# Performance work log

Hardware: AMD Instinct MI355X
Metric: run time of the kernel (lower is better)

## Reference

```python
import jax, jax.numpy as jnp
import numpy as np

D_MODEL, D_STATE, EXPAND, D_CONV, HEADDIM = 1024, 128, 2, 4, 64
D_INNER = EXPAND * D_MODEL                      # 2048
NHEADS = D_INNER // HEADDIM                     # 32
NGROUPS = 1
CONV_DIM = D_INNER + 2 * NGROUPS * D_STATE      # 2304
D_IN_PROJ = 2 * D_INNER + 2 * NGROUPS * D_STATE + NHEADS  # 4384
BATCH, SEQ = 2, 4096
EPS = 1e-5


def setup_inputs() -> dict:
    key = jax.random.key(0)
    ks = jax.random.split(key, 6)
    sn = lambda k, shape, sc: jax.random.normal(k, shape, jnp.float32) * sc
    # dt_bias such that softplus(dt_bias) spans [1e-3, 0.1] (mamba2 init)
    dt = jnp.linspace(1e-3, 0.1, NHEADS)
    return {
        "x": sn(ks[0], (BATCH, SEQ, D_MODEL), 1.0),
        "ln_w": jnp.ones((D_MODEL,), jnp.float32),
        "ln_b": jnp.zeros((D_MODEL,), jnp.float32),
        "in_proj_w": sn(ks[1], (D_IN_PROJ, D_MODEL), D_MODEL ** -0.5),
        "conv_w": sn(ks[2], (CONV_DIM, D_CONV), D_CONV ** -0.5),
        "conv_b": jnp.zeros((CONV_DIM,), jnp.float32),
        "dt_bias": jnp.log(jnp.expm1(dt)).astype(jnp.float32),
        "A_log": jnp.log(jnp.arange(1, NHEADS + 1, dtype=jnp.float32)),
        "D": jnp.ones((NHEADS,), jnp.float32),
        "norm_w": jnp.ones((D_INNER,), jnp.float32),
        "out_proj_w": sn(ks[3], (D_MODEL, D_INNER), D_INNER ** -0.5),
    }


def _mamba2(u, in_proj_w, conv_w, conv_b, dt_bias, A_log, Dp, norm_w, out_proj_w):
    b, l, _ = u.shape
    zxbcdt = u @ in_proj_w.T                              # [b,l,4384]
    z, xBC, dt = jnp.split(zxbcdt, [D_INNER, D_INNER + CONV_DIM], axis=-1)
    # causal depthwise conv1d over channels, then SiLU
    xBC = jnp.transpose(xBC, (0, 2, 1))                   # [b,conv_dim,l]
    xBC = jax.lax.conv_general_dilated(
        xBC, conv_w[:, None, :], window_strides=(1,),
        padding=[(D_CONV - 1, 0)], feature_group_count=CONV_DIM,
        dimension_numbers=("NCH", "OIH", "NCH"))
    xBC = jax.nn.silu(jnp.transpose(xBC, (0, 2, 1)) + conv_b)
    x, Bm, Cm = jnp.split(xBC, [D_INNER, D_INNER + NGROUPS * D_STATE], axis=-1)
    dt = jax.nn.softplus(dt + dt_bias)                    # [b,l,h]
    A = -jnp.exp(A_log)                                   # [h]
    xh = x.reshape(b, l, NHEADS, HEADDIM)
    # time-major for the selective scan
    dt_t, x_t = jnp.moveaxis(dt, 1, 0), jnp.moveaxis(xh, 1, 0)
    B_t, C_t = jnp.moveaxis(Bm, 1, 0), jnp.moveaxis(Cm, 1, 0)

    def step(h, inputs):
        dtk, xk, Bk, Ck = inputs                          # [b,h],[b,h,p],[b,n],[b,n]
        decay = jnp.exp(dtk * A)                          # [b,h]
        h = h * decay[:, :, None, None] + (dtk[:, :, None, None] * xk[..., None]) * Bk[:, None, None, :]
        y = jnp.einsum("bhpn,bn->bhp", h, Ck)
        return h, y

    h0 = jnp.zeros((b, NHEADS, HEADDIM, D_STATE), u.dtype)
    _, ys = jax.lax.scan(step, h0, (dt_t, x_t, B_t, C_t))  # ys: [l,b,h,p]
    y = jnp.moveaxis(ys, 0, 1) + Dp[None, None, :, None] * xh
    y = y.reshape(b, l, D_INNER)
    # gated RMSNorm: rmsnorm(y * silu(z)) * norm_w
    y = y * jax.nn.silu(z)
    y = y * jax.lax.rsqrt(jnp.mean(y * y, axis=-1, keepdims=True) + EPS) * norm_w
    return y @ out_proj_w.T


def reference(x, ln_w, ln_b, in_proj_w, conv_w, conv_b, dt_bias, A_log, D, norm_w, out_proj_w):
    mu = jnp.mean(x, -1, keepdims=True)
    var = jnp.mean((x - mu) ** 2, -1, keepdims=True)
    xn = (x - mu) * jax.lax.rsqrt(var + EPS) * ln_w + ln_b
    # dropout is identity at inference
    return x + _mamba2(xn, in_proj_w, conv_w, conv_b, dt_bias, A_log, D, norm_w, out_proj_w)
```

## Files before the change

kernel.cpp:

```cpp
#include <hip/hip_runtime.h>
#include <cstdint>

#define D_MODEL 1024
#define D_INNER 2048
#define NHEADS 32
#define HEADDIM 64
#define D_STATE 128
#define CONV_DIM 2304
#define D_IN_PROJ 4384
#define SEQ 4096
#define NROWS 8192
#define NPROJ_PAD 4480
#define TCH 128
#define NCHUNK 32
#define CR 8

typedef float f32x4 __attribute__((ext_vector_type(4)));
typedef __bf16 bf16x8 __attribute__((ext_vector_type(8)));
typedef unsigned short u16;

__device__ __forceinline__ u16 f2bf(float f) {
  uint32_t u = __builtin_bit_cast(uint32_t, f);
  u += 0x7FFFu + ((u >> 16) & 1u);
  return (u16)(u >> 16);
}
__device__ __forceinline__ float bf2f(u16 h) {
  return __builtin_bit_cast(float, (uint32_t)h << 16);
}
__device__ __forceinline__ float dexp(float a) { return expf(fminf(0.f, a)); }

typedef __attribute__((address_space(1))) const void gv_t;
typedef __attribute__((address_space(3))) void lv_t;
__device__ __forceinline__ void gload_lds16(const void* g, void* l) {
  __builtin_amdgcn_global_load_lds((gv_t*)g, (lv_t*)l, 16, 0, 0);
}

__global__ __launch_bounds__(256) void cvt_pad(const float* __restrict__ s,
                                               u16* __restrict__ d, int n_src, int n_dst) {
  int i = (blockIdx.x * 256 + threadIdx.x) * 4;
  int stride = gridDim.x * 256 * 4;
  for (; i < n_dst; i += stride) {
    ushort4 o;
    if (i < n_src) {
      float4 v = *(const float4*)&s[i];
      o.x = f2bf(v.x); o.y = f2bf(v.y); o.z = f2bf(v.z); o.w = f2bf(v.w);
    } else {
      o.x = o.y = o.z = o.w = 0;
    }
    *(ushort4*)&d[i] = o;
  }
}

__global__ __launch_bounds__(256) void ln_kernel(const float* __restrict__ x,
                                                 const float* __restrict__ w,
                                                 const float* __restrict__ b,
                                                 u16* __restrict__ out) {
  int row = blockIdx.x, tid = threadIdx.x;
  const float4 v = *(const float4*)&x[(long)row * D_MODEL + tid * 4];
  float s1 = v.x + v.y + v.z + v.w;
  float s2 = v.x * v.x + v.y * v.y + v.z * v.z + v.w * v.w;
#pragma unroll
  for (int m = 32; m >= 1; m >>= 1) {
    s1 += __shfl_xor(s1, m);
    s2 += __shfl_xor(s2, m);
  }
  __shared__ float p1[4], p2[4];
  if ((tid & 63) == 0) { p1[tid >> 6] = s1; p2[tid >> 6] = s2; }
  __syncthreads();
  s1 = p1[0] + p1[1] + p1[2] + p1[3];
  s2 = p2[0] + p2[1] + p2[2] + p2[3];
  float mean = s1 * (1.f / D_MODEL);
  float var = s2 * (1.f / D_MODEL) - mean * mean;
  float rstd = rsqrtf(var + 1e-5f);
  const float4 wv = *(const float4*)&w[tid * 4];
  const float4 bv = *(const float4*)&b[tid * 4];
  ushort4 o;
  o.x = f2bf((v.x - mean) * rstd * wv.x + bv.x);
  o.y = f2bf((v.y - mean) * rstd * wv.y + bv.y);
  o.z = f2bf((v.z - mean) * rstd * wv.z + bv.z);
  o.w = f2bf((v.w - mean) * rstd * wv.w + bv.w);
  *(ushort4*)&out[(long)row * D_MODEL + tid * 4] = o;
}

template <int MODE>
__global__ __launch_bounds__(256, 4) void gemm_bt(const u16* __restrict__ A,
                                                  const u16* __restrict__ B, int K,
                                                  u16* __restrict__ zb,
                                                  u16* __restrict__ xb,
                                                  float* __restrict__ dtb,
                                                  float* __restrict__ C,
                                                  const float* __restrict__ resid) {
  __shared__ __align__(16) u16 As[128 * 64];
  __shared__ __align__(16) u16 Bs[128 * 64];
  const int tid = threadIdx.x;
  const int NB = gridDim.x;
  const int wg = (blockIdx.x & 7) * (NB >> 3) + (blockIdx.x >> 3);
  const int m0 = (wg & 63) * 128;
  const int n0 = (wg >> 6) * 128;
  const int w = tid >> 6, l = tid & 63;
  const int wm = w >> 1, wn = w & 1;

  f32x4 acc[4][4] = {};

  for (int k0 = 0; k0 < K; k0 += 64) {
#pragma unroll
    for (int i = 0; i < 4; ++i) {
      int idx = i * 256 + tid;
      int row = idx >> 3, slot = idx & 7;
      int ks = slot ^ (row & 7);
      const u16* ga = A + (long)(m0 + row) * K + k0 + ks * 8;
      gload_lds16(ga, (char*)As + idx * 16);
      const u16* gb = B + (long)(n0 + row) * K + k0 + ks * 8;
      gload_lds16(gb, (char*)Bs + idx * 16);
    }
    __syncthreads();
    bf16x8 af[2][4], bfr[2][4];
#pragma unroll
    for (int kk = 0; kk < 2; ++kk)
#pragma unroll
      for (int f = 0; f < 4; ++f) {
        int rowa = wm * 64 + f * 16 + (l & 15);
        int ca = ((kk << 2) | (l >> 4)) ^ (rowa & 7);
        af[kk][f] = *(const bf16x8*)((const char*)As + rowa * 128 + ca * 16);
        int rowb = wn * 64 + f * 16 + (l & 15);
        int cb2 = ((kk << 2) | (l >> 4)) ^ (rowb & 7);
        bfr[kk][f] = *(const bf16x8*)((const char*)Bs + rowb * 128 + cb2 * 16);
      }
#pragma unroll
    for (int kk = 0; kk < 2; ++kk)
#pragma unroll
      for (int mf = 0; mf < 4; ++mf)
#pragma unroll
        for (int nf = 0; nf < 4; ++nf)
          acc[mf][nf] = __builtin_amdgcn_mfma_f32_16x16x32_bf16(
              af[kk][mf], bfr[kk][nf], acc[mf][nf], 0, 0, 0);
    __syncthreads();
  }
#pragma unroll
  for (int mf = 0; mf < 4; ++mf)
#pragma unroll
    for (int nf = 0; nf < 4; ++nf) {
      int col = n0 + wn * 64 + nf * 16 + (l & 15);
#pragma unroll
      for (int r = 0; r < 4; ++r) {
        int rowm = m0 + wm * 64 + mf * 16 + (l >> 4) * 4 + r;
        float v = acc[mf][nf][r];
        if (MODE == 0) {
          if (col < D_INNER)
            zb[(long)rowm * D_INNER + col] = f2bf(v);
          else if (col < D_INNER + CONV_DIM)
            xb[(long)rowm * CONV_DIM + (col - D_INNER)] = f2bf(v);
          else if (col < D_IN_PROJ)
            dtb[(long)rowm * NHEADS + (col - D_INNER - CONV_DIM)] = v;
        } else {
          long off = (long)rowm * D_MODEL + col;
          C[off] = v + resid[off];
        }
      }
    }
}

__global__ __launch_bounds__(256) void conv_silu_kernel(const u16* __restrict__ xr,
                                                        const float* __restrict__ cw,
                                                        const float* __restrict__ cb,
                                                        u16* __restrict__ xp,
                                                        u16* __restrict__ bc) {
  const int c = blockIdx.x * 256 + threadIdx.x;
  const int row0 = blockIdx.y * CR;
  const int t0 = row0 & (SEQ - 1);
  const float4 wv = *(const float4*)&cw[c * 4];
  const float bias = cb[c];
  float xwin[CR + 3];
#pragma unroll
  for (int k = 0; k < CR + 3; ++k) {
    int t = t0 - 3 + k;
    xwin[k] = (t >= 0) ? bf2f(xr[(long)(row0 - 3 + k) * CONV_DIM + c]) : 0.f;
  }
#pragma unroll
  for (int j = 0; j < CR; ++j) {
    float a = bias + xwin[j] * wv.x + xwin[j + 1] * wv.y + xwin[j + 2] * wv.z +
              xwin[j + 3] * wv.w;
    a = a / (1.f + expf(-a));
    int row = row0 + j;
    if (c < D_INNER)
      xp[(long)row * D_INNER + c] = f2bf(a);
    else
      bc[(long)row * (2 * D_STATE) + (c - D_INNER)] = f2bf(a);
  }
}

__global__ __launch_bounds__(256, 2) void ssd_state_kernel(
    const u16* __restrict__ xp, const u16* __restrict__ bcb,
    const float* __restrict__ dtf, const float* __restrict__ dt_bias,
    const float* __restrict__ A_log, u16* __restrict__ S,
    float* __restrict__ cdk) {
  const int hh = blockIdx.x, cc = blockIdx.y, bb = blockIdx.z;
  const int tid = threadIdx.x, w = tid >> 6, l = tid & 63;
  __shared__ __align__(16) u16 Bs[128 * 128];
  __shared__ __align__(16) u16 WXs[128 * 64];
  __shared__ float ws[128];
  const long rowbase = (long)bb * SEQ + cc * TCH;
  const float Ah = -expf(A_log[hh]);
  const float dbias = dt_bias[hh];

#pragma unroll
  for (int i = 0; i < 8; ++i) {
    int idx = i * 256 + tid, t = idx >> 4, kb = idx & 15;
    int kbs = kb ^ (((t >> 3) & 3) << 1);
    gload_lds16(bcb + (rowbase + t) * 256 + kbs * 8, (char*)Bs + idx * 16);
  }
  if (w == 0) {
    float r0 = dtf[(rowbase + l) * NHEADS + hh] + dbias;
    float r1 = dtf[(rowbase + 64 + l) * NHEADS + hh] + dbias;
    float d0 = r0 > 20.f ? r0 : log1pf(expf(r0));
    float d1 = r1 > 20.f ? r1 : log1pf(expf(r1));
    float a0 = d0 * Ah, a1 = d1 * Ah;
#pragma unroll
    for (int d = 1; d < 64; d <<= 1) { float u = __shfl_up(a0, d); if (l >= d) a0 += u; }
#pragma unroll
    for (int d = 1; d < 64; d <<= 1) { float u = __shfl_up(a1, d); if (l >= d) a1 += u; }
    float t0 = __shfl(a0, 63);
    float tot = __shfl(a1, 63) + t0;
    ws[l] = dexp(tot - a0) * d0;
    ws[64 + l] = dexp(tot - (a1 + t0)) * d1;
    if (l == 0) cdk[(bb * 32 + hh) * NCHUNK + cc] = dexp(tot);
  }
  __syncthreads();
#pragma unroll
  for (int i = 0; i < 4; ++i) {
    int sl = i * 256 + tid, t = sl >> 3, pb = sl & 7;
    bf16x8 v = *(const bf16x8*)&xp[(rowbase + t) * D_INNER + hh * 64 + pb * 8];
    float wt = ws[t];
    const u16* e = (const u16*)&v;
    u16 o[8];
#pragma unroll
    for (int j = 0; j < 8; ++j) o[j] = f2bf(bf2f(e[j]) * wt);
    *(bf16x8*)&WXs[t * 64 + ((pb * 8) ^ (((t >> 3) & 3) << 4))] = *(bf16x8*)o;
  }
  __syncthreads();

  f32x4 acc[8] = {};
  const int g4 = (l >> 4) << 4;
  const int p = w * 16 + (l & 15);
#pragma unroll
  for (int kc = 0; kc < 4; ++kc) {
    bf16x8 af;
#pragma unroll
    for (int j = 0; j < 8; ++j) {
      int t = kc * 32 + (l >> 4) * 8 + j;
      af[j] = __builtin_bit_cast(__bf16, WXs[t * 64 + (p ^ g4)]);
    }
#pragma unroll
    for (int nt = 0; nt < 8; ++nt) {
      int n = nt * 16 + (l & 15);
      bf16x8 bfv;
#pragma unroll
      for (int j = 0; j < 8; ++j) {
        int t = kc * 32 + (l >> 4) * 8 + j;
        bfv[j] = __builtin_bit_cast(__bf16, Bs[t * 128 + (n ^ g4)]);
      }
      acc[nt] = __builtin_amdgcn_mfma_f32_16x16x32_bf16(af, bfv, acc[nt], 0, 0, 0);
    }
  }
  u16* Sb = S + ((long)(bb * 32 + hh) * NCHUNK + cc) * 8192;
#pragma unroll
  for (int nt = 0; nt < 8; ++nt)
#pragma unroll
    for (int r = 0; r < 4; ++r) {
      int prow = w * 16 + (l >> 4) * 4 + r;
      Sb[prow * 128 + nt * 16 + (l & 15)] = f2bf(acc[nt][r]);
    }
}

__global__ __launch_bounds__(256) void ssd_combine(u16* __restrict__ SH,
                                                   const float* __restrict__ cdk) {
  const int hh = blockIdx.y, bb = blockIdx.z;
  const int pp = blockIdx.x * 16 + (threadIdx.x >> 4);
  const int nn = (threadIdx.x & 15) * 8;
  const int bh = bb * 32 + hh;
  u16* base = SH + (long)bh * NCHUNK * 8192 + pp * 128 + nn;
  const float* ck = cdk + bh * NCHUNK;
  float h[8] = {};
  for (int c = 0; c < NCHUNK; ++c) {
    bf16x8 sv = *(bf16x8*)(base + (long)c * 8192);
    const u16* se = (const u16*)&sv;
    u16 o[8];
#pragma unroll
    for (int j = 0; j < 8; ++j) o[j] = f2bf(h[j]);
    *(bf16x8*)(base + (long)c * 8192) = *(bf16x8*)o;
    float d = ck[c];
#pragma unroll
    for (int j = 0; j < 8; ++j) h[j] = fmaf(h[j], d, bf2f(se[j]));
  }
}

__global__ __launch_bounds__(256, 2) void ssd_y_kernel(
    const u16* __restrict__ xp, const u16* __restrict__ bcb,
    const float* __restrict__ dtf, const float* __restrict__ dt_bias,
    const float* __restrict__ A_log, const float* __restrict__ Dp,
    const u16* __restrict__ H, u16* __restrict__ y) {
  const int hh = blockIdx.x, cc = blockIdx.y, bb = blockIdx.z;
  const int tid = threadIdx.x, w = tid >> 6, l = tid & 63;
  __shared__ __align__(16) u16 Cs[128 * 128];
  __shared__ __align__(16) u16 Xs[128 * 64];
  __shared__ __align__(16) u16 Bp[32 * 128];
  __shared__ __align__(16) u16 Ms[128 * 40];
  __shared__ float sig[128], dts[128], esg[128];
  const long rowbase = (long)bb * SEQ + cc * TCH;
  const float Ah = -expf(A_log[hh]);
  const float Dh = Dp[hh];
  const float dbias = dt_bias[hh];

#pragma unroll
  for (int i = 0; i < 8; ++i) {
    int idx = i * 256 + tid, t = idx >> 4, sl = idx & 15;
    gload_lds16(bcb + (rowbase + t) * 256 + 128 + ((sl ^ (t & 15)) * 8),
                (char*)Cs + idx * 16);
  }
  if (w == 0) {
    float r0 = dtf[(rowbase + l) * NHEADS + hh] + dbias;
    float r1 = dtf[(rowbase + 64 + l) * NHEADS + hh] + dbias;
    float d0 = r0 > 20.f ? r0 : log1pf(expf(r0));
    float d1 = r1 > 20.f ? r1 : log1pf(expf(r1));
    float a0 = d0 * Ah, a1 = d1 * Ah;
#pragma unroll
    for (int d = 1; d < 64; d <<= 1) { float u = __shfl_up(a0, d); if (l >= d) a0 += u; }
#pragma unroll
    for (int d = 1; d < 64; d <<= 1) { float u = __shfl_up(a1, d); if (l >= d) a1 += u; }
    float t0 = __shfl(a0, 63);
    sig[l] = a0; sig[64 + l] = a1 + t0;
    dts[l] = d0; dts[64 + l] = d1;
    esg[l] = dexp(a0); esg[64 + l] = dexp(a1 + t0);
  }
#pragma unroll
  for (int i = 0; i < 4; ++i) {
    int sl = i * 256 + tid, t = sl >> 3, pb = sl & 7;
    bf16x8 v = *(const bf16x8*)&xp[(rowbase + t) * D_INNER + hh * 64 + pb * 8];
    *(bf16x8*)&Xs[t * 64 + ((pb * 8) ^ (((t >> 3) & 3) << 4))] = v;
  }
  __syncthreads();

  bf16x8 cfr[2][4];
#pragma unroll
  for (int tt = 0; tt < 2; ++tt) {
    int t = (w * 2 + tt) * 16 + (l & 15);
#pragma unroll
    for (int kc = 0; kc < 4; ++kc) {
      int sl = (kc * 4 + (l >> 4)) ^ (t & 15);
      cfr[tt][kc] = *(const bf16x8*)&Cs[t * 128 + sl * 8];
    }
  }
  f32x4 y1[2][4] = {};
  const int g4 = (l >> 4) << 4;

  for (int sp = 0; sp < 4; ++sp) {
    __syncthreads();
#pragma unroll
    for (int i = 0; i < 2; ++i) {
      int idx = i * 256 + tid, sr = idx >> 4, sl = idx & 15;
      gload_lds16(bcb + (rowbase + sp * 32 + sr) * 256 + ((sl ^ (sr & 15)) * 8),
                  (char*)Bp + idx * 16);
    }
    __syncthreads();
    f32x4 g[2][2] = {};
#pragma unroll
    for (int st = 0; st < 2; ++st)
#pragma unroll
      for (int kc = 0; kc < 4; ++kc) {
        int s = st * 16 + (l & 15);
        int sl = (kc * 4 + (l >> 4)) ^ (s & 15);
        bf16x8 bfv = *(const bf16x8*)&Bp[s * 128 + sl * 8];
        g[0][st] = __builtin_amdgcn_mfma_f32_16x16x32_bf16(cfr[0][kc], bfv, g[0][st], 0, 0, 0);
        g[1][st] = __builtin_amdgcn_mfma_f32_16x16x32_bf16(cfr[1][kc], bfv, g[1][st], 0, 0, 0);
      }
#pragma unroll
    for (int tt = 0; tt < 2; ++tt)
#pragma unroll
      for (int st = 0; st < 2; ++st)
#pragma unroll
        for (int r = 0; r < 4; ++r) {
          int t = (w * 2 + tt) * 16 + (l >> 4) * 4 + r;
          int s = sp * 32 + st * 16 + (l & 15);
          float m = 0.f;
          if (s <= t) m = g[tt][st][r] * dexp(sig[t] - sig[s]) * dts[s];
          Ms[t * 40 + st * 16 + (l & 15)] = f2bf(m);
        }
    __syncthreads();
#pragma unroll
    for (int tt = 0; tt < 2; ++tt) {
      int t = (w * 2 + tt) * 16 + (l & 15);
      bf16x8 mf = *(const bf16x8*)&Ms[t * 40 + (l >> 4) * 8];
#pragma unroll
      for (int pt = 0; pt < 4; ++pt) {
        int p = pt * 16 + (l & 15);
        bf16x8 xf;
#pragma unroll
        for (int j = 0; j < 8; ++j) {
          int s = sp * 32 + (l >> 4) * 8 + j;
          xf[j] = __builtin_bit_cast(__bf16, Xs[s * 64 + (p ^ g4)]);
        }
        y1[tt][pt] = __builtin_amdgcn_mfma_f32_16x16x32_bf16(mf, xf, y1[tt][pt], 0, 0, 0);
      }
    }
  }
  f32x4 y2[2][4] = {};
  const u16* Hb = H + ((long)(bb * 32 + hh) * NCHUNK + cc) * 8192;
#pragma unroll
  for (int pt = 0; pt < 4; ++pt) {
    int p = pt * 16 + (l & 15);
#pragma unroll
    for (int kc = 0; kc < 4; ++kc) {
      bf16x8 hf = *(const bf16x8*)&Hb[p * 128 + kc * 32 + (l >> 4) * 8];
      y2[0][pt] = __builtin_amdgcn_mfma_f32_16x16x32_bf16(cfr[0][kc], hf, y2[0][pt], 0, 0, 0);
      y2[1][pt] = __builtin_amdgcn_mfma_f32_16x16x32_bf16(cfr[1][kc], hf, y2[1][pt], 0, 0, 0);
    }
  }
#pragma unroll
  for (int tt = 0; tt < 2; ++tt)
#pragma unroll
    for (int pt = 0; pt < 4; ++pt)
#pragma unroll
      for (int r = 0; r < 4; ++r) {
        int t = (w * 2 + tt) * 16 + (l >> 4) * 4 + r;
        int p = pt * 16 + (l & 15);
        float xv = bf2f(Xs[t * 64 + (p ^ (((t >> 3) & 3) << 4))]);
        float yv = y1[tt][pt][r] + esg[t] * y2[tt][pt][r] + Dh * xv;
        y[(rowbase + t) * (long)D_INNER + hh * 64 + p] = f2bf(yv);
      }
}

__global__ __launch_bounds__(256) void grms_kernel(const u16* __restrict__ yb,
                                                   u16* __restrict__ zb,
                                                   const float* __restrict__ nw) {
  int row = blockIdx.x, tid = threadIdx.x;
  const u16* yp = yb + (long)row * D_INNER + tid * 8;
  u16* zp = zb + (long)row * D_INNER + tid * 8;
  ushort4 yv0 = *(const ushort4*)yp, yv1 = *(const ushort4*)(yp + 4);
  ushort4 zv0 = *(const ushort4*)zp, zv1 = *(const ushort4*)(zp + 4);
  u16 ya[8] = {yv0.x, yv0.y, yv0.z, yv0.w, yv1.x, yv1.y, yv1.z, yv1.w};
  u16 za[8] = {zv0.x, zv0.y, zv0.z, zv0.w, zv1.x, zv1.y, zv1.z, zv1.w};
  float g[8];
  float s2 = 0.f;
#pragma unroll
  for (int j = 0; j < 8; ++j) {
    float z = bf2f(za[j]);
    float gg = bf2f(ya[j]) * (z / (1.f + expf(-z)));
    g[j] = gg;
    s2 += gg * gg;
  }
#pragma unroll
  for (int m = 32; m >= 1; m >>= 1) s2 += __shfl_xor(s2, m);
  __shared__ float p2[4];
  if ((tid & 63) == 0) p2[tid >> 6] = s2;
  __syncthreads();
  s2 = p2[0] + p2[1] + p2[2] + p2[3];
  float r = rsqrtf(s2 * (1.f / D_INNER) + 1e-5f);
  const float4 w0 = *(const float4*)&nw[tid * 8];
  const float4 w1 = *(const float4*)&nw[tid * 8 + 4];
  const float* wp = (const float*)&w0;
  const float* wq = (const float*)&w1;
  ushort4 o0, o1;
  o0.x = f2bf(g[0] * r * wp[0]); o0.y = f2bf(g[1] * r * wp[1]);
  o0.z = f2bf(g[2] * r * wp[2]); o0.w = f2bf(g[3] * r * wp[3]);
  o1.x = f2bf(g[4] * r * wq[0]); o1.y = f2bf(g[5] * r * wq[1]);
  o1.z = f2bf(g[6] * r * wq[2]); o1.w = f2bf(g[7] * r * wq[3]);
  *(ushort4*)zp = o0;
  *(ushort4*)(zp + 4) = o1;
}

extern "C" void kernel_launch(void* const* d_in, const int* in_sizes, int n_in,
                              void* d_out, int out_size, void* d_ws, size_t ws_size,
                              hipStream_t stream) {
  const float* x = (const float*)d_in[0];
  const float* ln_w = (const float*)d_in[1];
  const float* ln_b = (const float*)d_in[2];
  const float* in_proj_w = (const float*)d_in[3];
  const float* conv_w = (const float*)d_in[4];
  const float* conv_b = (const float*)d_in[5];
  const float* dt_bias = (const float*)d_in[6];
  const float* A_log = (const float*)d_in[7];
  const float* Dvec = (const float*)d_in[8];
  const float* norm_w = (const float*)d_in[9];
  const float* out_proj_w = (const float*)d_in[10];
  float* out = (float*)d_out;

  char* ws = (char*)d_ws;
  u16* W2bf = (u16*)(ws + 0);
  u16* zbf = (u16*)(ws + 4194304);
  u16* xpart = (u16*)(ws + 37748736);
  u16* bcbf = (u16*)(ws + 71303168);
  float* dtf = (float*)(ws + 75497472);
  float* cdk = (float*)(ws + 76546048);
  u16* W1bf = (u16*)(ws + 76554240);
  u16* xbcraw = (u16*)(ws + 85729280);
  u16* SH = (u16*)(ws + 76554240);
  u16* xnbf = (u16*)d_out;
  u16* ybf = (u16*)d_out;

  cvt_pad<<<512, 256, 0, stream>>>(in_proj_w, W1bf, D_IN_PROJ * D_MODEL,
                                   NPROJ_PAD * D_MODEL);
  cvt_pad<<<512, 256, 0, stream>>>(out_proj_w, W2bf, D_MODEL * D_INNER,
                                   D_MODEL * D_INNER);
  ln_kernel<<<NROWS, 256, 0, stream>>>(x, ln_w, ln_b, xnbf);
  gemm_bt<0><<<35 * 64, 256, 0, stream>>>(xnbf, W1bf, D_MODEL, zbf, xbcraw, dtf,
                                          nullptr, nullptr);
  conv_silu_kernel<<<dim3(9, NROWS / CR), 256, 0, stream>>>(xbcraw, conv_w, conv_b,
                                                            xpart, bcbf);
  ssd_state_kernel<<<dim3(32, NCHUNK, 2), 256, 0, stream>>>(xpart, bcbf, dtf, dt_bias,
                                                            A_log, SH, cdk);
  ssd_combine<<<dim3(4, 32, 2), 256, 0, stream>>>(SH, cdk);
  ssd_y_kernel<<<dim3(32, NCHUNK, 2), 256, 0, stream>>>(xpart, bcbf, dtf, dt_bias,
                                                        A_log, Dvec, SH, ybf);
  grms_kernel<<<NROWS, 256, 0, stream>>>(ybf, zbf, norm_w);
  gemm_bt<1><<<8 * 64, 256, 0, stream>>>(zbf, W2bf, D_INNER, nullptr, nullptr,
                                         nullptr, out, x);
}
```

Measured before the change: 324.4 us.

## Transpose SSD operands into padded LDS and load MFMA fragments directly from global

The state kernel now stores B and weighted X transposed in padded (pitch 136) shared memory, so MFMA operand fragments become single 16-byte LDS reads instead of eight scalar gathers. The y kernel drops the C and B staging buffers, reads C and B fragments straight from global memory, and computes the full 128x128 masked decay matrix in one pass rather than four 32-column slices with barriers. Launch bounds rise to three blocks per CU, and the chunk-combine loop prefetches the next chunk's state. The transposing scalar LDS stores and uncached global fragment reads may cost more than the gathers they replace, and the larger g accumulator array raises register pressure against the higher occupancy target.

```diff
diff --git a/kernel.cpp b/kernel.cpp
--- a/kernel.cpp
+++ b/kernel.cpp
@@ -14,6 +14,7 @@
 #define TCH 128
 #define NCHUNK 32
 #define CR 8
+#define PITCH 136
 
 typedef float f32x4 __attribute__((ext_vector_type(4)));
 typedef __bf16 bf16x8 __attribute__((ext_vector_type(8)));
@@ -189,26 +190,20 @@
   }
 }
 
-__global__ __launch_bounds__(256, 2) void ssd_state_kernel(
+__global__ __launch_bounds__(256, 3) void ssd_state_kernel(
     const u16* __restrict__ xp, const u16* __restrict__ bcb,
     const float* __restrict__ dtf, const float* __restrict__ dt_bias,
     const float* __restrict__ A_log, u16* __restrict__ S,
     float* __restrict__ cdk) {
   const int hh = blockIdx.x, cc = blockIdx.y, bb = blockIdx.z;
   const int tid = threadIdx.x, w = tid >> 6, l = tid & 63;
-  __shared__ __align__(16) u16 Bs[128 * 128];
-  __shared__ __align__(16) u16 WXs[128 * 64];
+  __shared__ __align__(16) u16 BT[128 * PITCH];
+  __shared__ __align__(16) u16 WXT[64 * PITCH];
   __shared__ float ws[128];
   const long rowbase = (long)bb * SEQ + cc * TCH;
   const float Ah = -expf(A_log[hh]);
   const float dbias = dt_bias[hh];
 
-#pragma unroll
-  for (int i = 0; i < 8; ++i) {
-    int idx = i * 256 + tid, t = idx >> 4, kb = idx & 15;
-    int kbs = kb ^ (((t >> 3) & 3) << 1);
-    gload_lds16(bcb + (rowbase + t) * 256 + kbs * 8, (char*)Bs + idx * 16);
-  }
   if (w == 0) {
     float r0 = dtf[(rowbase + l) * NHEADS + hh] + dbias;
     float r1 = dtf[(rowbase + 64 + l) * NHEADS + hh] + dbias;
@@ -225,6 +220,14 @@
     ws[64 + l] = dexp(tot - (a1 + t0)) * d1;
     if (l == 0) cdk[(bb * 32 + hh) * NCHUNK + cc] = dexp(tot);
   }
+#pragma unroll
+  for (int i = 0; i < 8; ++i) {
+    int idx = i * 256 + tid, t = idx >> 4, kb = idx & 15;
+    bf16x8 v = *(const bf16x8*)&bcb[(rowbase + t) * 256 + kb * 8];
+    const u16* e = (const u16*)&v;
+#pragma unroll
+    for (int j = 0; j < 8; ++j) BT[(kb * 8 + j) * PITCH + t] = e[j];
+  }
   __syncthreads();
 #pragma unroll
   for (int i = 0; i < 4; ++i) {
@@ -232,33 +235,21 @@
     bf16x8 v = *(const bf16x8*)&xp[(rowbase + t) * D_INNER + hh * 64 + pb * 8];
     float wt = ws[t];
     const u16* e = (const u16*)&v;
-    u16 o[8];
-#pragma unroll
-    for (int j = 0; j < 8; ++j) o[j] = f2bf(bf2f(e[j]) * wt);
-    *(bf16x8*)&WXs[t * 64 + ((pb * 8) ^ (((t >> 3) & 3) << 4))] = *(bf16x8*)o;
+#pragma unroll
+    for (int j = 0; j < 8; ++j)
+      WXT[(pb * 8 + j) * PITCH + t] = f2bf(bf2f(e[j]) * wt);
   }
   __syncthreads();
 
   f32x4 acc[8] = {};
-  const int g4 = (l >> 4) << 4;
   const int p = w * 16 + (l & 15);
 #pragma unroll
   for (int kc = 0; kc < 4; ++kc) {
-    bf16x8 af;
-#pragma unroll
-    for (int j = 0; j < 8; ++j) {
-      int t = kc * 32 + (l >> 4) * 8 + j;
-      af[j] = __builtin_bit_cast(__bf16, WXs[t * 64 + (p ^ g4)]);
-    }
+    bf16x8 af = *(const bf16x8*)&WXT[p * PITCH + kc * 32 + (l >> 4) * 8];
 #pragma unroll
     for (int nt = 0; nt < 8; ++nt) {
       int n = nt * 16 + (l & 15);
-      bf16x8 bfv;
-#pragma unroll
-      for (int j = 0; j < 8; ++j) {
-        int t = kc * 32 + (l >> 4) * 8 + j;
-        bfv[j] = __builtin_bit_cast(__bf16, Bs[t * 128 + (n ^ g4)]);
-      }
+      bf16x8 bfv = *(const bf16x8*)&BT[n * PITCH + kc * 32 + (l >> 4) * 8];
       acc[nt] = __builtin_amdgcn_mfma_f32_16x16x32_bf16(af, bfv, acc[nt], 0, 0, 0);
     }
   }
@@ -281,9 +272,11 @@
   u16* base = SH + (long)bh * NCHUNK * 8192 + pp * 128 + nn;
   const float* ck = cdk + bh * NCHUNK;
   float h[8] = {};
+  bf16x8 cur = *(bf16x8*)base;
   for (int c = 0; c < NCHUNK; ++c) {
-    bf16x8 sv = *(bf16x8*)(base + (long)c * 8192);
-    const u16* se = (const u16*)&sv;
+    bf16x8 nxt = cur;
+    if (c + 1 < NCHUNK) nxt = *(bf16x8*)(base + (long)(c + 1) * 8192);
+    const u16* se = (const u16*)&cur;
     u16 o[8];
 #pragma unroll
     for (int j = 0; j < 8; ++j) o[j] = f2bf(h[j]);
@@ -291,32 +284,25 @@
     float d = ck[c];
 #pragma unroll
     for (int j = 0; j < 8; ++j) h[j] = fmaf(h[j], d, bf2f(se[j]));
-  }
-}
-
-__global__ __launch_bounds__(256, 2) void ssd_y_kernel(
+    cur = nxt;
+  }
+}
+
+__global__ __launch_bounds__(256, 3) void ssd_y_kernel(
     const u16* __restrict__ xp, const u16* __restrict__ bcb,
     const float* __restrict__ dtf, const float* __restrict__ dt_bias,
     const float* __restrict__ A_log, const float* __restrict__ Dp,
     const u16* __restrict__ H, u16* __restrict__ y) {
   const int hh = blockIdx.x, cc = blockIdx.y, bb = blockIdx.z;
   const int tid = threadIdx.x, w = tid >> 6, l = tid & 63;
-  __shared__ __align__(16) u16 Cs[128 * 128];
-  __shared__ __align__(16) u16 Xs[128 * 64];
-  __shared__ __align__(16) u16 Bp[32 * 128];
-  __shared__ __align__(16) u16 Ms[128 * 40];
+  __shared__ __align__(16) u16 XT[64 * PITCH];
+  __shared__ __align__(16) u16 Ms[128 * PITCH];
   __shared__ float sig[128], dts[128], esg[128];
   const long rowbase = (long)bb * SEQ + cc * TCH;
   const float Ah = -expf(A_log[hh]);
   const float Dh = Dp[hh];
   const float dbias = dt_bias[hh];
 
-#pragma unroll
-  for (int i = 0; i < 8; ++i) {
-    int idx = i * 256 + tid, t = idx >> 4, sl = idx & 15;
-    gload_lds16(bcb + (rowbase + t) * 256 + 128 + ((sl ^ (t & 15)) * 8),
-                (char*)Cs + idx * 16);
-  }
   if (w == 0) {
     float r0 = dtf[(rowbase + l) * NHEADS + hh] + dbias;
     float r1 = dtf[(rowbase + 64 + l) * NHEADS + hh] + dbias;
@@ -336,7 +322,9 @@
   for (int i = 0; i < 4; ++i) {
     int sl = i * 256 + tid, t = sl >> 3, pb = sl & 7;
     bf16x8 v = *(const bf16x8*)&xp[(rowbase + t) * D_INNER + hh * 64 + pb * 8];
-    *(bf16x8*)&Xs[t * 64 + ((pb * 8) ^ (((t >> 3) & 3) << 4))] = v;
+    const u16* e = (const u16*)&v;
+#pragma unroll
+    for (int j = 0; j < 8; ++j) XT[(pb * 8 + j) * PITCH + t] = e[j];
   }
   __syncthreads();
 
@@ -345,62 +333,48 @@
   for (int tt = 0; tt < 2; ++tt) {
     int t = (w * 2 + tt) * 16 + (l & 15);
 #pragma unroll
+    for (int kc = 0; kc < 4; ++kc)
+      cfr[tt][kc] = *(const bf16x8*)&bcb[(rowbase + t) * 256 + 128 + kc * 32 +
+                                         (l >> 4) * 8];
+  }
+  f32x4 g[2][8] = {};
+#pragma unroll
+  for (int st = 0; st < 8; ++st) {
+    int s = st * 16 + (l & 15);
+#pragma unroll
     for (int kc = 0; kc < 4; ++kc) {
-      int sl = (kc * 4 + (l >> 4)) ^ (t & 15);
-      cfr[tt][kc] = *(const bf16x8*)&Cs[t * 128 + sl * 8];
-    }
-  }
+      bf16x8 bfv = *(const bf16x8*)&bcb[(rowbase + s) * 256 + kc * 32 + (l >> 4) * 8];
+      g[0][st] = __builtin_amdgcn_mfma_f32_16x16x32_bf16(cfr[0][kc], bfv, g[0][st], 0, 0, 0);
+      g[1][st] = __builtin_amdgcn_mfma_f32_16x16x32_bf16(cfr[1][kc], bfv, g[1][st], 0, 0, 0);
+    }
+  }
+#pragma unroll
+  for (int tt = 0; tt < 2; ++tt)
+#pragma unroll
+    for (int st = 0; st < 8; ++st)
+#pragma unroll
+      for (int r = 0; r < 4; ++r) {
+        int t = (w * 2 + tt) * 16 + (l >> 4) * 4 + r;
+        int s = st * 16 + (l & 15);
+        float m = 0.f;
+        if (s <= t) m = g[tt][st][r] * dexp(sig[t] - sig[s]) * dts[s];
+        Ms[t * PITCH + s] = f2bf(m);
+      }
+  __syncthreads();
+
   f32x4 y1[2][4] = {};
-  const int g4 = (l >> 4) << 4;
-
-  for (int sp = 0; sp < 4; ++sp) {
-    __syncthreads();
-#pragma unroll
-    for (int i = 0; i < 2; ++i) {
-      int idx = i * 256 + tid, sr = idx >> 4, sl = idx & 15;
-      gload_lds16(bcb + (rowbase + sp * 32 + sr) * 256 + ((sl ^ (sr & 15)) * 8),
-                  (char*)Bp + idx * 16);
-    }
-    __syncthreads();
-    f32x4 g[2][2] = {};
-#pragma unroll
-    for (int st = 0; st < 2; ++st)
-#pragma unroll
-      for (int kc = 0; kc < 4; ++kc) {
-        int s = st * 16 + (l & 15);
-        int sl = (kc * 4 + (l >> 4)) ^ (s & 15);
-        bf16x8 bfv = *(const bf16x8*)&Bp[s * 128 + sl * 8];
-        g[0][st] = __builtin_amdgcn_mfma_f32_16x16x32_bf16(cfr[0][kc], bfv, g[0][st], 0, 0, 0);
-        g[1][st] = __builtin_amdgcn_mfma_f32_16x16x32_bf16(cfr[1][kc], bfv, g[1][st], 0, 0, 0);
-      }
-#pragma unroll
-    for (int tt = 0; tt < 2; ++tt)
-#pragma unroll
-      for (int st = 0; st < 2; ++st)
-#pragma unroll
-        for (int r = 0; r < 4; ++r) {
-          int t = (w * 2 + tt) * 16 + (l >> 4) * 4 + r;
-          int s = sp * 32 + st * 16 + (l & 15);
-          float m = 0.f;
-          if (s <= t) m = g[tt][st][r] * dexp(sig[t] - sig[s]) * dts[s];
-          Ms[t * 40 + st * 16 + (l & 15)] = f2bf(m);
-        }
-    __syncthreads();
-#pragma unroll
-    for (int tt = 0; tt < 2; ++tt) {
-      int t = (w * 2 + tt) * 16 + (l & 15);
-      bf16x8 mf = *(const bf16x8*)&Ms[t * 40 + (l >> 4) * 8];
-#pragma unroll
-      for (int pt = 0; pt < 4; ++pt) {
-        int p = pt * 16 + (l & 15);
-        bf16x8 xf;
-#pragma unroll
-        for (int j = 0; j < 8; ++j) {
-          int s = sp * 32 + (l >> 4) * 8 + j;
-          xf[j] = __builtin_bit_cast(__bf16, Xs[s * 64 + (p ^ g4)]);
-        }
-        y1[tt][pt] = __builtin_amdgcn_mfma_f32_16x16x32_bf16(mf, xf, y1[tt][pt], 0, 0, 0);
-      }
+  const int t0r = (w * 2) * 16 + (l & 15);
+  const int t1r = (w * 2 + 1) * 16 + (l & 15);
+#pragma unroll
+  for (int kc = 0; kc < 4; ++kc) {
+    bf16x8 mf0 = *(const bf16x8*)&Ms[t0r * PITCH + kc * 32 + (l >> 4) * 8];
+    bf16x8 mf1 = *(const bf16x8*)&Ms[t1r * PITCH + kc * 32 + (l >> 4) * 8];
+#pragma unroll
+    for (int pt = 0; pt < 4; ++pt) {
+      int p = pt * 16 + (l & 15);
+      bf16x8 xf = *(const bf16x8*)&XT[p * PITCH + kc * 32 + (l >> 4) * 8];
+      y1[0][pt] = __builtin_amdgcn_mfma_f32_16x16x32_bf16(mf0, xf, y1[0][pt], 0, 0, 0);
+      y1[1][pt] = __builtin_amdgcn_mfma_f32_16x16x32_bf16(mf1, xf, y1[1][pt], 0, 0, 0);
     }
   }
   f32x4 y2[2][4] = {};
@@ -423,7 +397,7 @@
       for (int r = 0; r < 4; ++r) {
         int t = (w * 2 + tt) * 16 + (l >> 4) * 4 + r;
         int p = pt * 16 + (l & 15);
-        float xv = bf2f(Xs[t * 64 + (p ^ (((t >> 3) & 3) << 4))]);
+        float xv = bf2f(XT[p * PITCH + t]);
         float yv = y1[tt][pt][r] + esg[t] * y2[tt][pt][r] + Dh * xv;
         y[(rowbase + t) * (long)D_INNER + hh * 64 + p] = f2bf(yv);
       }
```

New measurement: 359.1 us. +10.7%, slower.
